# Performance work log

Measured on AMD Instinct MI355X. Metric: run time of the kernel, lower is better.

## Reference

```python
import jax, jax.numpy as jnp
import numpy as np
from jax import lax

B, S, L = 128, 256, 10
WORD, CHAR = 50000, 100
TAGS, START, END = 32, 30, 31
WDIM, CDIM, FILT, H = 100, 30, 30, 100
LSTM_IN = WDIM + FILT  # 130
NEG = -10000.0


def setup_inputs() -> dict:
    key = jax.random.key(0)
    ks = jax.random.split(key, 24)
    sc = 0.1
    word_emb = (jax.random.normal(ks[0], (WORD, WDIM), jnp.float32) * sc).at[0].set(0.0)  # padding_idx=0
    char_emb = (jax.random.normal(ks[1], (CHAR, CDIM), jnp.float32) * sc).at[0].set(0.0)
    conv_w = jax.random.normal(ks[2], (FILT, 1, 3, CDIM), jnp.float32) * sc  # OIHW, kernel (3, char_dim)
    conv_b = jax.random.normal(ks[3], (FILT,), jnp.float32) * sc
    wih_f = jax.random.normal(ks[4], (4 * H, LSTM_IN), jnp.float32) * sc
    whh_f = jax.random.normal(ks[5], (4 * H, H), jnp.float32) * sc
    bih_f = jax.random.normal(ks[6], (4 * H,), jnp.float32) * sc
    bhh_f = jax.random.normal(ks[7], (4 * H,), jnp.float32) * sc
    wih_b = jax.random.normal(ks[8], (4 * H, LSTM_IN), jnp.float32) * sc
    whh_b = jax.random.normal(ks[9], (4 * H, H), jnp.float32) * sc
    bih_b = jax.random.normal(ks[10], (4 * H,), jnp.float32) * sc
    bhh_b = jax.random.normal(ks[11], (4 * H,), jnp.float32) * sc
    proj_w = jax.random.normal(ks[12], (TAGS, 2 * H), jnp.float32) * sc
    proj_b = jax.random.normal(ks[13], (TAGS,), jnp.float32) * sc
    trans = jax.random.normal(ks[14], (TAGS, TAGS), jnp.float32)
    trans = trans.at[:, START].set(NEG).at[END, :].set(NEG)  # CRF.reset_parm
    word_x = jax.random.randint(ks[15], (B, S), 1, WORD, jnp.int32)
    char_x = jax.random.randint(ks[16], (B, S, L), 1, CHAR, jnp.int32)
    y = jax.random.randint(ks[17], (B, S), 0, 30, jnp.int32)  # gold tags exclude start/end
    mask = jnp.ones((B, S), jnp.int32)
    return dict(word_emb=word_emb, char_emb=char_emb, conv_w=conv_w, conv_b=conv_b,
                wih_f=wih_f, whh_f=whh_f, bih_f=bih_f, bhh_f=bhh_f,
                wih_b=wih_b, whh_b=whh_b, bih_b=bih_b, bhh_b=bhh_b,
                proj_w=proj_w, proj_b=proj_b, trans=trans,
                word_x=word_x, char_x=char_x, y=y, mask=mask)


def _lstm_dir(x, wih, whh, bih, bhh, reverse):
    # x: [B, S, D] -> hidden states [B, S, H]; PyTorch gate order i, f, g, o
    b = bih + bhh
    xs = jnp.swapaxes(x, 0, 1)  # [S, B, D]
    if reverse:
        xs = xs[::-1]
    Bv = x.shape[0]
    Hd = whh.shape[1]
    init = (jnp.zeros((Bv, Hd), x.dtype), jnp.zeros((Bv, Hd), x.dtype))
    def step(carry, xt):
        h, c = carry
        g = xt @ wih.T + h @ whh.T + b  # [B, 4H]
        i, f, gg, o = jnp.split(g, 4, axis=-1)
        c = jax.nn.sigmoid(f) * c + jax.nn.sigmoid(i) * jnp.tanh(gg)
        h = jax.nn.sigmoid(o) * jnp.tanh(c)
        return (h, c), h
    _, hs = lax.scan(step, init, xs)
    if reverse:
        hs = hs[::-1]
    return jnp.swapaxes(hs, 0, 1)


def _forward(word_emb, char_emb, conv_w, conv_b, wih_f, whh_f, bih_f, bhh_f,
             wih_b, whh_b, bih_b, bhh_b, proj_w, proj_b, trans,
             word_x, char_x, y, mask):
    # --- CharCNN (dropout = identity in eval) ---
    ce = char_emb[char_x].reshape(B * S, 1, L, CDIM)  # [B*S, 1, L, CDIM]
    fm = lax.conv_general_dilated(ce, conv_w, (1, 1), ((2, 2), (0, 0)),
                                  dimension_numbers=('NCHW', 'OIHW', 'NCHW'))
    fm = fm + conv_b[None, :, None, None]  # [B*S, FILT, L+2, 1]
    char_feat = fm.max(axis=(2, 3)).reshape(B, S, FILT)
    # --- BiLSTM + projection ---
    x = jnp.concatenate([word_emb[word_x], char_feat], axis=-1)  # [B, S, 130]
    h_f = _lstm_dir(x, wih_f, whh_f, bih_f, bhh_f, False)
    h_b = _lstm_dir(x, wih_b, whh_b, bih_b, bhh_b, True)
    emission = jnp.concatenate([h_f, h_b], axis=-1) @ proj_w.T + proj_b  # [B, S, TAGS]
    maskf = mask.astype(emission.dtype)
    # --- CRF gold-path score (vectorized form of compute_y_score) ---
    y_pad = jnp.concatenate([jnp.full((B, 1), START, y.dtype), y], axis=1)  # [B, S+1]
    prev, cur = y_pad[:, :-1], y_pad[:, 1:]
    p = jnp.take_along_axis(emission, cur[..., None].astype(jnp.int32), axis=-1)[..., 0]
    t = trans[prev, cur]
    score_y = ((p + t) * maskf).sum(axis=1) + trans[y[:, -1], END]  # original uses last label unmasked
    # --- CRF partition function (logsumexp scan over time) ---
    la0 = jnp.full((B, TAGS), NEG, emission.dtype).at[:, START].set(0.0)
    def step(la, em_m):
        em, m = em_m  # em: [B, TAGS], m: [B]
        la2 = jax.nn.logsumexp(la[:, :, None] + trans[None, :, :] + em[:, None, :], axis=1)
        m = m[:, None]
        return la2 * m + la * (1.0 - m), None
    la, _ = lax.scan(step, la0, (jnp.swapaxes(emission, 0, 1), maskf.T))
    la = la + trans[:, END][None, :]
    total = jax.nn.logsumexp(la, axis=1, keepdims=True)  # [B, 1]
    # faithful to original: [B] - [B,1] broadcasts to [B,B], then mean
    return -jnp.mean(score_y - total)


def reference(word_emb, char_emb, conv_w, conv_b, wih_f, whh_f, bih_f, bhh_f,
              wih_b, whh_b, bih_b, bhh_b, proj_w, proj_b, trans,
              word_x, char_x, y, mask):
    return _forward(word_emb, char_emb, conv_w, conv_b, wih_f, whh_f, bih_f, bhh_f,
                    wih_b, whh_b, bih_b, bhh_b, proj_w, proj_b, trans,
                    word_x, char_x, y, mask)
```

## Files before the change

### kernel.cpp

```cpp
#include <hip/hip_runtime.h>
#include <hip/hip_fp16.h>
#include <cstdint>
#include <cstddef>

#define BB 128
#define SS 256
#define LL 10
#define NTAGS 32
#define TAG_START 30
#define TAG_END 31
#define WDIM 100
#define CDIM 30
#define NFILT 30
#define HDIM 100
#define KIN 130
#define KPAD 160
#define GDIM 400
#define NROWS 832
#define NEGV -10000.0f
#define CTOK 8

#define NB_CONV (BB * SS / CTOK)
#define NB_WORD (BB * SS * KPAD / 256)
#define NB_WCVT (NROWS * KPAD / 256)
#define NB_PRE  (NB_CONV + NB_WORD + NB_WCVT)

typedef _Float16 h2 __attribute__((ext_vector_type(2)));
typedef _Float16 f16x8 __attribute__((ext_vector_type(8)));
typedef float f32x4 __attribute__((ext_vector_type(4)));

#if __has_builtin(__builtin_amdgcn_fdot2)
#define HAVE_FDOT2 1
#else
#define HAVE_FDOT2 0
#endif

__device__ __forceinline__ float sigm(float x) { return 1.0f / (1.0f + __expf(-x)); }
__device__ __forceinline__ float tanh_fast(float x) { return 2.0f / (1.0f + __expf(-2.0f * x)) - 1.0f; }

__device__ __forceinline__ void barrier_lds_only() {
  asm volatile("s_waitcnt lgkmcnt(0)" ::: "memory");
  __builtin_amdgcn_s_barrier();
  asm volatile("" ::: "memory");
}

__global__ __launch_bounds__(256) void k_pre(
    const float* __restrict__ wemb, const int* __restrict__ wx,
    const float* __restrict__ cemb, const float* __restrict__ convw,
    const float* __restrict__ convb, const int* __restrict__ cx,
    const float* __restrict__ wihF, const float* __restrict__ wihB,
    _Float16* __restrict__ x16, _Float16* __restrict__ w16,
    float* __restrict__ out) {
  int blk = blockIdx.x;
  int tid = threadIdx.x;
  if (blk == 0 && tid == 0) out[0] = 0.f;

  if (blk < NB_CONV) {
    int tok8 = tid >> 5;
    int f = tid & 31;
    int token0 = blk * CTOK;
    __shared__ float e[CTOK][LL * CDIM];
    __shared__ float cw[NFILT * 3 * CDIM];
    __shared__ float cb[NFILT];
    __shared__ int ci[CTOK][LL];
    if (tid < CTOK * LL) {
      int t = tid / LL, l = tid - t * LL;
      ci[t][l] = cx[(token0 + t) * LL + l];
    }
    for (int i = tid; i < NFILT * 3 * CDIM; i += 256) cw[i] = convw[i];
    if (tid < NFILT) cb[tid] = convb[tid];
    __syncthreads();
    for (int i = tid; i < CTOK * LL * CDIM; i += 256) {
      int t = i / (LL * CDIM);
      int r = i - t * (LL * CDIM);
      int l = r / CDIM, c = r - l * CDIM;
      e[t][l * CDIM + c] = cemb[ci[t][l] * CDIM + c];
    }
    __syncthreads();
    if (f < NFILT) {
      float d0[LL], d1[LL], d2[LL];
#pragma unroll
      for (int l = 0; l < LL; l++) { d0[l] = 0.f; d1[l] = 0.f; d2[l] = 0.f; }
      const float* et = &e[tok8][0];
      for (int c = 0; c < CDIM; c++) {
        float w0 = cw[(f * 3 + 0) * CDIM + c];
        float w1 = cw[(f * 3 + 1) * CDIM + c];
        float w2 = cw[(f * 3 + 2) * CDIM + c];
#pragma unroll
        for (int l = 0; l < LL; l++) {
          float ev = et[l * CDIM + c];
          d0[l] += ev * w0; d1[l] += ev * w1; d2[l] += ev * w2;
        }
      }
      float bias = cb[f];
      float m = -3.0e38f;
#pragma unroll
      for (int h = 0; h < LL + 2; h++) {
        float acc = bias;
        int j0 = h - 2, j1 = h - 1, j2 = h;
        if (j0 >= 0 && j0 < LL) acc += d0[j0];
        if (j1 >= 0 && j1 < LL) acc += d1[j1];
        if (j2 >= 0 && j2 < LL) acc += d2[j2];
        m = fmaxf(m, acc);
      }
      x16[(size_t)(token0 + tok8) * KPAD + WDIM + f] = (_Float16)m;
    }
  } else if (blk < NB_CONV + NB_WORD) {
    int idx = (blk - NB_CONV) * 256 + tid;
    int token = idx / KPAD;
    int d = idx - token * KPAD;
    if (d < WDIM) {
      x16[idx] = (_Float16)wemb[(size_t)wx[token] * WDIM + d];
    } else if (d >= KIN) {
      x16[idx] = (_Float16)0.f;
    }
  } else {
    int idx = (blk - NB_CONV - NB_WORD) * 256 + tid;
    int n = idx / KPAD;
    int k = idx - n * KPAD;
    float v = 0.f;
    if (k < KIN && n < 2 * GDIM) {
      v = (n < GDIM) ? wihF[(size_t)n * KIN + k] : wihB[(size_t)(n - GDIM) * KIN + k];
    }
    w16[idx] = (_Float16)v;
  }
}

__global__ __launch_bounds__(256) void k_pregemm(
    const _Float16* __restrict__ x16, const _Float16* __restrict__ w16,
    const float* __restrict__ bihF, const float* __restrict__ bhhF,
    const float* __restrict__ bihB, const float* __restrict__ bhhB,
    _Float16* __restrict__ preF, _Float16* __restrict__ preB) {
  __shared__ __align__(16) _Float16 Asl[64 * 40];
  __shared__ __align__(16) _Float16 Bsl[64 * 40];
  int m0 = blockIdx.x * 64;
  int n0 = blockIdx.y * 64;
  int tid = threadIdx.x;
  int lane = tid & 63, w = tid >> 6;
  int quad = lane >> 4, l15 = lane & 15;

  f32x4 acc[4];
#pragma unroll
  for (int i = 0; i < 4; i++) acc[i] = (f32x4){0.f, 0.f, 0.f, 0.f};

  int r = tid >> 2;
  int kk = (tid & 3) * 8;
  const _Float16* xs = x16 + (size_t)(m0 + r) * KPAD + kk;
  const _Float16* wsrc = w16 + (size_t)(n0 + r) * KPAD + kk;

  for (int kc = 0; kc < 5; kc++) {
    if (kc) __syncthreads();
    *(f16x8*)&Asl[r * 40 + kk] = *(const f16x8*)(xs + kc * 32);
    *(f16x8*)&Bsl[r * 40 + kk] = *(const f16x8*)(wsrc + kc * 32);
    __syncthreads();

    f16x8 bfrag = *(const f16x8*)&Bsl[(w * 16 + l15) * 40 + quad * 8];
#pragma unroll
    for (int mt = 0; mt < 4; mt++) {
      f16x8 afrag = *(const f16x8*)&Asl[(mt * 16 + l15) * 40 + quad * 8];
      acc[mt] = __builtin_amdgcn_mfma_f32_16x16x32_f16(afrag, bfrag, acc[mt], 0, 0, 0);
    }
  }

  int ng = n0 + w * 16 + l15;
  if (ng < 2 * GDIM) {
    int dir = ng >= GDIM;
    int jb = dir ? ng - GDIM : ng;
    _Float16* dst = dir ? preB : preF;
    float bias = (dir ? bihB : bihF)[jb] + (dir ? bhhB : bhhF)[jb];
#pragma unroll
    for (int mt = 0; mt < 4; mt++) {
#pragma unroll
      for (int i = 0; i < 4; i++) {
        int m = m0 + mt * 16 + quad * 4 + i;
        dst[(size_t)m * GDIM + jb] = (_Float16)(acc[mt][i] + bias);
      }
    }
  }
}

#define CH 32
#define NCH (SS / CH)
__global__ __launch_bounds__(256, 1) void k_lstm(
    const _Float16* __restrict__ preF, const _Float16* __restrict__ preB,
    const float* __restrict__ whhF, const float* __restrict__ whhB,
    _Float16* __restrict__ hbuf) {
  int blk = blockIdx.x;
  int dir = blk >> 7;
  int b = blk & 127;
  const _Float16* pre = dir ? preB : preF;
  const float* whh = dir ? whhB : whhF;
  int tid = threadIdx.x;
  int j = tid >> 1;
  int kh = tid & 1;
  bool act = (j < HDIM);
  int jc = act ? j : 0;

  __half2 wp[4][25];
#pragma unroll
  for (int g = 0; g < 4; g++) {
    const float* wr = whh + (size_t)(g * HDIM + jc) * HDIM + kh * 50;
#pragma unroll
    for (int q = 0; q < 25; q++) {
      wp[g][q] = __floats2half2_rn(wr[2 * q], wr[2 * q + 1]);
    }
  }

  __shared__ __align__(16) _Float16 preS[14336];
  __shared__ __align__(16) _Float16 hsh[2][2][64];
  if (tid < 128) ((int*)hsh)[tid] = 0;
  float c = 0.f;

#define GSRC(ck) ((const uint4*)(pre + ((size_t)b * SS + (dir ? (SS - CH - (ck) * CH) : ((ck) * CH))) * GDIM))

  uint4 r0, r1, r2, r3, r4, r5, r6;
  {
    const uint4* s0 = GSRC(0);
    r0 = s0[0 * 256 + tid]; r1 = s0[1 * 256 + tid]; r2 = s0[2 * 256 + tid];
    r3 = s0[3 * 256 + tid]; r4 = s0[4 * 256 + tid]; r5 = s0[5 * 256 + tid];
    r6 = s0[6 * 256 + tid];
  }

  _Float16* hptr = hbuf + ((size_t)b * SS + (dir ? (SS - 1) : 0)) * (2 * HDIM) + dir * HDIM + jc;
  const intptr_t hstep = dir ? -(intptr_t)(2 * HDIM) : (intptr_t)(2 * HDIM);

  int cur = 0;
  for (int ck = 0; ck < NCH; ck++) {
    asm volatile("s_waitcnt vmcnt(0)" ::: "memory");
    *(uint4*)&preS[(0 * 256 + tid) * 8] = r0;
    *(uint4*)&preS[(1 * 256 + tid) * 8] = r1;
    *(uint4*)&preS[(2 * 256 + tid) * 8] = r2;
    *(uint4*)&preS[(3 * 256 + tid) * 8] = r3;
    *(uint4*)&preS[(4 * 256 + tid) * 8] = r4;
    *(uint4*)&preS[(5 * 256 + tid) * 8] = r5;
    *(uint4*)&preS[(6 * 256 + tid) * 8] = r6;
    if (ck + 1 < NCH) {
      const uint4* snx = GSRC(ck + 1);
      r0 = snx[0 * 256 + tid]; r1 = snx[1 * 256 + tid]; r2 = snx[2 * 256 + tid];
      r3 = snx[3 * 256 + tid]; r4 = snx[4 * 256 + tid]; r5 = snx[5 * 256 + tid];
      r6 = snx[6 * 256 + tid];
    }
    barrier_lds_only();

    int preOff = (dir ? (CH - 1) * GDIM : 0) + kh * 200 + jc;
    const int pdelta = dir ? -GDIM : GDIM;

    for (int s2 = 0; s2 < CH; s2++) {
      float paF = (float)preS[preOff];
      float pbF = (float)preS[preOff + 100];

      const _Float16* hseg = &hsh[cur][kh][0];
      uint4 hv0 = *(const uint4*)(hseg);
      uint4 hv1 = *(const uint4*)(hseg + 8);
      uint4 hv2 = *(const uint4*)(hseg + 16);
      uint4 hv3 = *(const uint4*)(hseg + 24);
      uint4 hv4 = *(const uint4*)(hseg + 32);
      uint4 hv5 = *(const uint4*)(hseg + 40);
      uint32_t hv6 = *(const uint32_t*)(hseg + 48);
      __half2 hp[25];
      hp[0]  = __builtin_bit_cast(__half2, hv0.x);
      hp[1]  = __builtin_bit_cast(__half2, hv0.y);
      hp[2]  = __builtin_bit_cast(__half2, hv0.z);
      hp[3]  = __builtin_bit_cast(__half2, hv0.w);
      hp[4]  = __builtin_bit_cast(__half2, hv1.x);
      hp[5]  = __builtin_bit_cast(__half2, hv1.y);
      hp[6]  = __builtin_bit_cast(__half2, hv1.z);
      hp[7]  = __builtin_bit_cast(__half2, hv1.w);
      hp[8]  = __builtin_bit_cast(__half2, hv2.x);
      hp[9]  = __builtin_bit_cast(__half2, hv2.y);
      hp[10] = __builtin_bit_cast(__half2, hv2.z);
      hp[11] = __builtin_bit_cast(__half2, hv2.w);
      hp[12] = __builtin_bit_cast(__half2, hv3.x);
      hp[13] = __builtin_bit_cast(__half2, hv3.y);
      hp[14] = __builtin_bit_cast(__half2, hv3.z);
      hp[15] = __builtin_bit_cast(__half2, hv3.w);
      hp[16] = __builtin_bit_cast(__half2, hv4.x);
      hp[17] = __builtin_bit_cast(__half2, hv4.y);
      hp[18] = __builtin_bit_cast(__half2, hv4.z);
      hp[19] = __builtin_bit_cast(__half2, hv4.w);
      hp[20] = __builtin_bit_cast(__half2, hv5.x);
      hp[21] = __builtin_bit_cast(__half2, hv5.y);
      hp[22] = __builtin_bit_cast(__half2, hv5.z);
      hp[23] = __builtin_bit_cast(__half2, hv5.w);
      hp[24] = __builtin_bit_cast(__half2, hv6);

      float racc[4];
#if HAVE_FDOT2
#pragma unroll
      for (int g = 0; g < 4; g++) {
        float a0 = 0.f, a1 = 0.f;
#pragma unroll
        for (int q = 0; q < 25; q += 2)
          a0 = __builtin_amdgcn_fdot2(__builtin_bit_cast(h2, wp[g][q]),
                                      __builtin_bit_cast(h2, hp[q]), a0, false);
#pragma unroll
        for (int q = 1; q < 25; q += 2)
          a1 = __builtin_amdgcn_fdot2(__builtin_bit_cast(h2, wp[g][q]),
                                      __builtin_bit_cast(h2, hp[q]), a1, false);
        racc[g] = a0 + a1;
      }
#else
      __half2 z = __floats2half2_rn(0.f, 0.f);
#pragma unroll
      for (int g = 0; g < 4; g++) {
        __half2 a0 = z, a1 = z;
#pragma unroll
        for (int q = 0; q < 25; q += 2) a0 = __hfma2(wp[g][q], hp[q], a0);
#pragma unroll
        for (int q = 1; q < 25; q += 2) a1 = __hfma2(wp[g][q], hp[q], a1);
        racc[g] = (__low2float(a0) + __high2float(a0)) +
                  (__low2float(a1) + __high2float(a1));
      }
#endif

      if (kh == 0) { racc[0] += paF; racc[1] += pbF; }
      else         { racc[2] += paF; racc[3] += pbF; }
#pragma unroll
      for (int g = 0; g < 4; g++) racc[g] += __shfl_xor(racc[g], 1);

      float ig = sigm(racc[0]), fg = sigm(racc[1]);
      float g2 = tanh_fast(racc[2]), og = sigm(racc[3]);
      c = fg * c + ig * g2;
      float h = og * tanh_fast(c);

      if (act && kh == 0) {
        int seg = (j >= 50) ? 1 : 0;
        hsh[cur ^ 1][seg][j - seg * 50] = (_Float16)h;
        *hptr = (_Float16)h;
      }

      barrier_lds_only();
      cur ^= 1;
      preOff += pdelta;
      hptr += hstep;
    }
  }
#undef GSRC
}

__global__ __launch_bounds__(256) void k_proj(const _Float16* __restrict__ hbuf,
                                              const float* __restrict__ pw,
                                              const float* __restrict__ pb,
                                              float* __restrict__ em) {
  __shared__ __align__(16) float pws[NTAGS * 204];
  __shared__ float pbs[NTAGS];
  int tid = threadIdx.x;
  for (int i = tid; i < NTAGS * 2 * HDIM; i += 256) {
    int tag = i / (2 * HDIM);
    int k = i - tag * (2 * HDIM);
    pws[tag * 204 + k] = pw[i];
  }
  if (tid < NTAGS) pbs[tid] = pb[tid];
  __syncthreads();

  int idx = blockIdx.x * blockDim.x + tid;
  if (idx >= BB * SS * NTAGS) return;
  int token = idx >> 5, tag = idx & 31;
  const uint4* h4 = (const uint4*)(hbuf + (size_t)token * 2 * HDIM);
  const float4* w4 = (const float4*)&pws[tag * 204];
  float acc = pbs[tag];
#pragma unroll
  for (int k = 0; k < 25; k++) {
    uint4 hv = h4[k];
    h2 a = __builtin_bit_cast(h2, hv.x);
    h2 bq = __builtin_bit_cast(h2, hv.y);
    h2 cq = __builtin_bit_cast(h2, hv.z);
    h2 d = __builtin_bit_cast(h2, hv.w);
    float4 w0 = w4[k * 2], w1 = w4[k * 2 + 1];
    acc += (float)a.x * w0.x + (float)a.y * w0.y + (float)bq.x * w0.z + (float)bq.y * w0.w
         + (float)cq.x * w1.x + (float)cq.y * w1.y + (float)d.x * w1.z + (float)d.y * w1.w;
  }
  em[idx] = acc;
}

__global__ __launch_bounds__(64) void k_crf(const float* __restrict__ em,
                                            const float* __restrict__ trans,
                                            const int* __restrict__ mask,
                                            const int* __restrict__ y,
                                            float* __restrict__ out) {
  int b = blockIdx.x;
  int lane = threadIdx.x;
  int j = lane & 31;
  int h = lane >> 5;

  __shared__ __align__(16) float emS[SS * NTAGS];
  __shared__ __align__(16) int mkS[SS];
  {
    const uint4* src = (const uint4*)(em + (size_t)b * SS * NTAGS);
#pragma unroll
    for (int p = 0; p < 32; p++) {
      uint4 t = src[p * 64 + lane];
      *(uint4*)&emS[(p * 64 + lane) * 4] = t;
    }
    uint4 mv = ((const uint4*)(mask + (size_t)b * SS))[lane];
    *(uint4*)&mkS[lane * 4] = mv;
  }
  barrier_lds_only();

  float sacc = 0.f;
  for (int s = lane; s < SS; s += 64) {
    int curt = y[b * SS + s];
    int prevt = (s == 0) ? TAG_START : y[b * SS + s - 1];
    float mk = (float)mkS[s];
    sacc += (emS[s * NTAGS + curt] + trans[prevt * NTAGS + curt]) * mk;
  }
#pragma unroll
  for (int off = 32; off > 0; off >>= 1) sacc += __shfl_down(sacc, off);
  float scoreYv = __shfl(sacc, 0) + trans[y[b * SS + SS - 1] * NTAGS + TAG_END];

  float tcol[16];
#pragma unroll
  for (int i = 0; i < 16; i++) tcol[i] = trans[(h * 16 + i) * NTAGS + j];

  float la = (j == TAG_START) ? 0.f : NEGV;

  for (int s = 0; s < SS; s++) {
    float e0 = emS[s * NTAGS + j];
    float mkv = (float)mkS[s];

    float v[16];
#pragma unroll
    for (int i = 0; i < 16; i++) v[i] = __shfl(la, h * 16 + i) + tcol[i];

    float ma = v[0], mb2 = v[1];
#pragma unroll
    for (int i = 2; i < 16; i += 2) { ma = fmaxf(ma, v[i]); mb2 = fmaxf(mb2, v[i + 1]); }
    float mh = fmaxf(ma, mb2);
    float m = fmaxf(mh, __shfl_xor(mh, 32));

    float sa = 0.f, sb = 0.f;
#pragma unroll
    for (int i = 0; i < 16; i += 2) { sa += __expf(v[i] - m); sb += __expf(v[i + 1] - m); }
    float sh = sa + sb;
    float sum = sh + __shfl_xor(sh, 32);

    float la2 = m + __logf(sum) + e0;
    la = la2 * mkv + la * (1.f - mkv);
  }
  la += trans[j * NTAGS + TAG_END];

  float mm = la;
#pragma unroll
  for (int off = 16; off > 0; off >>= 1) mm = fmaxf(mm, __shfl_xor(mm, off));
  float ss = __expf(la - mm);
#pragma unroll
  for (int off = 16; off > 0; off >>= 1) ss += __shfl_xor(ss, off);
  float total = mm + __logf(ss);
  if (lane == 0) atomicAdd(out, (total - scoreYv) * (1.0f / BB));
}

extern "C" void kernel_launch(void* const* d_in, const int* in_sizes, int n_in,
                              void* d_out, int out_size, void* d_ws, size_t ws_size,
                              hipStream_t stream) {
  const float* word_emb = (const float*)d_in[0];
  const float* char_emb = (const float*)d_in[1];
  const float* conv_w   = (const float*)d_in[2];
  const float* conv_b   = (const float*)d_in[3];
  const float* wih_f    = (const float*)d_in[4];
  const float* whh_f    = (const float*)d_in[5];
  const float* bih_f    = (const float*)d_in[6];
  const float* bhh_f    = (const float*)d_in[7];
  const float* wih_b    = (const float*)d_in[8];
  const float* whh_b    = (const float*)d_in[9];
  const float* bih_b    = (const float*)d_in[10];
  const float* bhh_b    = (const float*)d_in[11];
  const float* proj_w   = (const float*)d_in[12];
  const float* proj_b   = (const float*)d_in[13];
  const float* trans    = (const float*)d_in[14];
  const int* word_x     = (const int*)d_in[15];
  const int* char_x     = (const int*)d_in[16];
  const int* y          = (const int*)d_in[17];
  const int* mask       = (const int*)d_in[18];
  float* out = (float*)d_out;

  _Float16* x16   = (_Float16*)d_ws;
  _Float16* w16   = x16 + (size_t)BB * SS * KPAD;
  _Float16* preF  = w16 + (size_t)NROWS * KPAD;
  _Float16* preB  = preF + (size_t)BB * SS * GDIM;
  _Float16* hbuf  = preB + (size_t)BB * SS * GDIM;
  float* em       = (float*)(hbuf + (size_t)BB * SS * 2 * HDIM);

  k_pre<<<NB_PRE, 256, 0, stream>>>(word_emb, word_x, char_emb, conv_w, conv_b,
                                    char_x, wih_f, wih_b, x16, w16, out);
  k_pregemm<<<dim3(BB * SS / 64, 13), 256, 0, stream>>>(x16, w16, bih_f, bhh_f,
                                                        bih_b, bhh_b, preF, preB);
  k_lstm<<<256, 256, 0, stream>>>(preF, preB, whh_f, whh_b, hbuf);
  k_proj<<<(BB * SS * NTAGS + 255) / 256, 256, 0, stream>>>(hbuf, proj_w, proj_b, em);
  k_crf<<<BB, 64, 0, stream>>>(em, trans, mask, y, out);
}
```

Baseline: 495.2 us.

## Restructure input GEMM tiling, vectorize embedding gather, swap CRF shuffles for LDS, drop fdot2

The input-projection GEMM now keeps the whole 64-row A tile resident in LDS and loops over all 13 N tiles, double-buffering the weight tile so the next one loads while the current one computes. This replaces a 2D grid that reloaded A for every N tile. The word-embedding gather is split into vectorized 8-element float4 loads plus a small tail and padding pass. The CRF recurrence broadcasts the alpha vector through LDS with float4 reads instead of 16 cross-lane shuffles, and the LSTM always uses the half2 hfma path instead of fdot2. The GEMM grid shrinks to one block per 64-row tile, which lowers parallelism and raises LDS use. The LDS broadcast in the CRF relies on single-wave ordering and has no barrier.

```diff
diff --git a/kernel.cpp b/kernel.cpp
--- a/kernel.cpp
+++ b/kernel.cpp
@@ -21,19 +21,14 @@
 #define CTOK 8
 
 #define NB_CONV (BB * SS / CTOK)
-#define NB_WORD (BB * SS * KPAD / 256)
+#define NB_WORDA (BB * SS * 12 / 256)
+#define NB_WORDB (BB * SS * 20 / 256)
 #define NB_WCVT (NROWS * KPAD / 256)
-#define NB_PRE  (NB_CONV + NB_WORD + NB_WCVT)
+#define NB_PRE  (NB_CONV + NB_WORDA + NB_WORDB + NB_WCVT)
 
 typedef _Float16 h2 __attribute__((ext_vector_type(2)));
 typedef _Float16 f16x8 __attribute__((ext_vector_type(8)));
 typedef float f32x4 __attribute__((ext_vector_type(4)));
-
-#if __has_builtin(__builtin_amdgcn_fdot2)
-#define HAVE_FDOT2 1
-#else
-#define HAVE_FDOT2 0
-#endif
 
 __device__ __forceinline__ float sigm(float x) { return 1.0f / (1.0f + __expf(-x)); }
 __device__ __forceinline__ float tanh_fast(float x) { return 2.0f / (1.0f + __expf(-2.0f * x)) - 1.0f; }
@@ -105,17 +100,30 @@
       }
       x16[(size_t)(token0 + tok8) * KPAD + WDIM + f] = (_Float16)m;
     }
-  } else if (blk < NB_CONV + NB_WORD) {
+  } else if (blk < NB_CONV + NB_WORDA) {
     int idx = (blk - NB_CONV) * 256 + tid;
-    int token = idx / KPAD;
-    int d = idx - token * KPAD;
-    if (d < WDIM) {
-      x16[idx] = (_Float16)wemb[(size_t)wx[token] * WDIM + d];
-    } else if (d >= KIN) {
-      x16[idx] = (_Float16)0.f;
+    int token = idx / 12;
+    int g = idx - token * 12;
+    const float* src = wemb + (size_t)wx[token] * WDIM + g * 8;
+    float4 f0 = *(const float4*)(src);
+    float4 f1 = *(const float4*)(src + 4);
+    f16x8 v;
+    v[0] = (_Float16)f0.x; v[1] = (_Float16)f0.y;
+    v[2] = (_Float16)f0.z; v[3] = (_Float16)f0.w;
+    v[4] = (_Float16)f1.x; v[5] = (_Float16)f1.y;
+    v[6] = (_Float16)f1.z; v[7] = (_Float16)f1.w;
+    *(f16x8*)&x16[(size_t)token * KPAD + g * 8] = v;
+  } else if (blk < NB_CONV + NB_WORDA + NB_WORDB) {
+    int idx = (blk - NB_CONV - NB_WORDA) * 256 + tid;
+    int token = idx / 20;
+    int u = idx - token * 20;
+    if (u < 4) {
+      x16[(size_t)token * KPAD + 96 + u] = (_Float16)wemb[(size_t)wx[token] * WDIM + 96 + u];
+    } else if (u < 19) {
+      *(uint32_t*)&x16[(size_t)token * KPAD + KIN + 2 * (u - 4)] = 0;
     }
   } else {
-    int idx = (blk - NB_CONV - NB_WORD) * 256 + tid;
+    int idx = (blk - NB_CONV - NB_WORDA - NB_WORDB) * 256 + tid;
     int n = idx / KPAD;
     int k = idx - n * KPAD;
     float v = 0.f;
@@ -131,50 +139,74 @@
     const float* __restrict__ bihF, const float* __restrict__ bhhF,
     const float* __restrict__ bihB, const float* __restrict__ bhhB,
     _Float16* __restrict__ preF, _Float16* __restrict__ preB) {
-  __shared__ __align__(16) _Float16 Asl[64 * 40];
-  __shared__ __align__(16) _Float16 Bsl[64 * 40];
+  __shared__ __align__(16) _Float16 Asl[64 * 168];
+  __shared__ __align__(16) _Float16 Bsl[2][64 * 168];
   int m0 = blockIdx.x * 64;
-  int n0 = blockIdx.y * 64;
   int tid = threadIdx.x;
   int lane = tid & 63, w = tid >> 6;
   int quad = lane >> 4, l15 = lane & 15;
-
-  f32x4 acc[4];
-#pragma unroll
-  for (int i = 0; i < 4; i++) acc[i] = (f32x4){0.f, 0.f, 0.f, 0.f};
-
   int r = tid >> 2;
   int kk = (tid & 3) * 8;
+
   const _Float16* xs = x16 + (size_t)(m0 + r) * KPAD + kk;
-  const _Float16* wsrc = w16 + (size_t)(n0 + r) * KPAD + kk;
-
+  const _Float16* ws = w16 + (size_t)r * KPAD + kk;
+#pragma unroll
   for (int kc = 0; kc < 5; kc++) {
-    if (kc) __syncthreads();
-    *(f16x8*)&Asl[r * 40 + kk] = *(const f16x8*)(xs + kc * 32);
-    *(f16x8*)&Bsl[r * 40 + kk] = *(const f16x8*)(wsrc + kc * 32);
-    __syncthreads();
-
-    f16x8 bfrag = *(const f16x8*)&Bsl[(w * 16 + l15) * 40 + quad * 8];
-#pragma unroll
-    for (int mt = 0; mt < 4; mt++) {
-      f16x8 afrag = *(const f16x8*)&Asl[(mt * 16 + l15) * 40 + quad * 8];
-      acc[mt] = __builtin_amdgcn_mfma_f32_16x16x32_f16(afrag, bfrag, acc[mt], 0, 0, 0);
-    }
-  }
-
-  int ng = n0 + w * 16 + l15;
-  if (ng < 2 * GDIM) {
-    int dir = ng >= GDIM;
-    int jb = dir ? ng - GDIM : ng;
-    _Float16* dst = dir ? preB : preF;
-    float bias = (dir ? bihB : bihF)[jb] + (dir ? bhhB : bhhF)[jb];
-#pragma unroll
-    for (int mt = 0; mt < 4; mt++) {
-#pragma unroll
-      for (int i = 0; i < 4; i++) {
-        int m = m0 + mt * 16 + quad * 4 + i;
-        dst[(size_t)m * GDIM + jb] = (_Float16)(acc[mt][i] + bias);
+    *(f16x8*)&Asl[r * 168 + kc * 32 + kk] = *(const f16x8*)(xs + kc * 32);
+    *(f16x8*)&Bsl[0][r * 168 + kc * 32 + kk] = *(const f16x8*)(ws + kc * 32);
+  }
+  __syncthreads();
+
+  for (int nt = 0; nt < 13; nt++) {
+    int cur = nt & 1;
+    f16x8 nb0, nb1, nb2, nb3, nb4;
+    if (nt + 1 < 13) {
+      const _Float16* wn = w16 + (size_t)((nt + 1) * 64 + r) * KPAD + kk;
+      nb0 = *(const f16x8*)(wn);
+      nb1 = *(const f16x8*)(wn + 32);
+      nb2 = *(const f16x8*)(wn + 64);
+      nb3 = *(const f16x8*)(wn + 96);
+      nb4 = *(const f16x8*)(wn + 128);
+    }
+
+    f32x4 acc[4];
+#pragma unroll
+    for (int i = 0; i < 4; i++) acc[i] = (f32x4){0.f, 0.f, 0.f, 0.f};
+#pragma unroll
+    for (int kc = 0; kc < 5; kc++) {
+      f16x8 bfrag = *(const f16x8*)&Bsl[cur][(w * 16 + l15) * 168 + kc * 32 + quad * 8];
+#pragma unroll
+      for (int mt = 0; mt < 4; mt++) {
+        f16x8 afrag = *(const f16x8*)&Asl[(mt * 16 + l15) * 168 + kc * 32 + quad * 8];
+        acc[mt] = __builtin_amdgcn_mfma_f32_16x16x32_f16(afrag, bfrag, acc[mt], 0, 0, 0);
       }
+    }
+
+    int ng = nt * 64 + w * 16 + l15;
+    if (ng < 2 * GDIM) {
+      int dir = ng >= GDIM;
+      int jb = dir ? ng - GDIM : ng;
+      _Float16* dst = dir ? preB : preF;
+      float bias = (dir ? bihB : bihF)[jb] + (dir ? bhhB : bhhF)[jb];
+#pragma unroll
+      for (int mt = 0; mt < 4; mt++) {
+#pragma unroll
+        for (int i = 0; i < 4; i++) {
+          int m = m0 + mt * 16 + quad * 4 + i;
+          dst[(size_t)m * GDIM + jb] = (_Float16)(acc[mt][i] + bias);
+        }
+      }
+    }
+
+    if (nt + 1 < 13) {
+      asm volatile("s_waitcnt vmcnt(0)" ::: "memory");
+      int nxt = cur ^ 1;
+      *(f16x8*)&Bsl[nxt][r * 168 + 0 * 32 + kk] = nb0;
+      *(f16x8*)&Bsl[nxt][r * 168 + 1 * 32 + kk] = nb1;
+      *(f16x8*)&Bsl[nxt][r * 168 + 2 * 32 + kk] = nb2;
+      *(f16x8*)&Bsl[nxt][r * 168 + 3 * 32 + kk] = nb3;
+      *(f16x8*)&Bsl[nxt][r * 168 + 4 * 32 + kk] = nb4;
+      __syncthreads();
     }
   }
 }
@@ -285,21 +317,6 @@
       hp[24] = __builtin_bit_cast(__half2, hv6);
 
       float racc[4];
-#if HAVE_FDOT2
-#pragma unroll
-      for (int g = 0; g < 4; g++) {
-        float a0 = 0.f, a1 = 0.f;
-#pragma unroll
-        for (int q = 0; q < 25; q += 2)
-          a0 = __builtin_amdgcn_fdot2(__builtin_bit_cast(h2, wp[g][q]),
-                                      __builtin_bit_cast(h2, hp[q]), a0, false);
-#pragma unroll
-        for (int q = 1; q < 25; q += 2)
-          a1 = __builtin_amdgcn_fdot2(__builtin_bit_cast(h2, wp[g][q]),
-                                      __builtin_bit_cast(h2, hp[q]), a1, false);
-        racc[g] = a0 + a1;
-      }
-#else
       __half2 z = __floats2half2_rn(0.f, 0.f);
 #pragma unroll
       for (int g = 0; g < 4; g++) {
@@ -311,7 +328,6 @@
         racc[g] = (__low2float(a0) + __high2float(a0)) +
                   (__low2float(a1) + __high2float(a1));
       }
-#endif
 
       if (kh == 0) { racc[0] += paF; racc[1] += pbF; }
       else         { racc[2] += paF; racc[3] += pbF; }
@@ -385,6 +401,7 @@
 
   __shared__ __align__(16) float emS[SS * NTAGS];
   __shared__ __align__(16) int mkS[SS];
+  __shared__ __align__(16) float laS[2][32];
   {
     const uint4* src = (const uint4*)(em + (size_t)b * SS * NTAGS);
 #pragma unroll
@@ -418,9 +435,20 @@
     float e0 = emS[s * NTAGS + j];
     float mkv = (float)mkS[s];
 
+    if (lane < 32) laS[s & 1][lane] = la;
+    asm volatile("s_waitcnt lgkmcnt(0)" ::: "memory");
+    const float4* lp = (const float4*)&laS[s & 1][h * 16];
+    float4 t0 = lp[0], t1 = lp[1], t2 = lp[2], t3 = lp[3];
+
     float v[16];
-#pragma unroll
-    for (int i = 0; i < 16; i++) v[i] = __shfl(la, h * 16 + i) + tcol[i];
+    v[0] = t0.x + tcol[0];  v[1] = t0.y + tcol[1];
+    v[2] = t0.z + tcol[2];  v[3] = t0.w + tcol[3];
+    v[4] = t1.x + tcol[4];  v[5] = t1.y + tcol[5];
+    v[6] = t1.z + tcol[6];  v[7] = t1.w + tcol[7];
+    v[8] = t2.x + tcol[8];  v[9] = t2.y + tcol[9];
+    v[10] = t2.z + tcol[10]; v[11] = t2.w + tcol[11];
+    v[12] = t3.x + tcol[12]; v[13] = t3.y + tcol[13];
+    v[14] = t3.z + tcol[14]; v[15] = t3.w + tcol[15];
 
     float ma = v[0], mb2 = v[1];
 #pragma unroll
@@ -482,8 +510,8 @@
 
   k_pre<<<NB_PRE, 256, 0, stream>>>(word_emb, word_x, char_emb, conv_w, conv_b,
                                     char_x, wih_f, wih_b, x16, w16, out);
-  k_pregemm<<<dim3(BB * SS / 64, 13), 256, 0, stream>>>(x16, w16, bih_f, bhh_f,
-                                                        bih_b, bhh_b, preF, preB);
+  k_pregemm<<<BB * SS / 64, 256, 0, stream>>>(x16, w16, bih_f, bhh_f,
+                                              bih_b, bhh_b, preF, preB);
   k_lstm<<<256, 256, 0, stream>>>(preF, preB, whh_f, whh_b, hbuf);
   k_proj<<<(BB * SS * NTAGS + 255) / 256, 256, 0, stream>>>(hbuf, proj_w, proj_b, em);
   k_crf<<<BB, 64, 0, stream>>>(em, trans, mask, y, out);
```

Measured after the change: 483.4 us. 2.4% less time.
